# Performance work log

Hardware: AMD Instinct MI355X
Metric: run time of the kernel (lower is better)

The kernel has to match this reference:

```python
import jax, jax.numpy as jnp
import numpy as np

B_TAIL = 3.0  # 'bins' arg = tail bound of the spline interval [-B, B]


def _rqs_forward(u, w, h, d):
    """Rational-quadratic spline (Durkan et al.) with linear (identity) tails.
    u: (batch, dim); w,h: (dim, K); d: (dim, K-1). Returns x (batch, dim), logdet (batch,)."""
    dim, K = w.shape
    two_b = 2.0 * B_TAIL

    widths = jax.nn.softmax(w, axis=-1) * two_b                      # (dim, K)
    cum_w = jnp.concatenate(
        [jnp.full((dim, 1), -B_TAIL, u.dtype), -B_TAIL + jnp.cumsum(widths, axis=-1)],
        axis=-1)                                                     # (dim, K+1) knot x-positions
    cum_w = cum_w.at[:, -1].set(B_TAIL)

    heights = jax.nn.softmax(h, axis=-1) * two_b                     # (dim, K)
    cum_h = jnp.concatenate(
        [jnp.full((dim, 1), -B_TAIL, u.dtype), -B_TAIL + jnp.cumsum(heights, axis=-1)],
        axis=-1)                                                     # (dim, K+1) knot y-positions
    cum_h = cum_h.at[:, -1].set(B_TAIL)

    ones = jnp.ones((dim, 1), u.dtype)
    derivs = jnp.concatenate([ones, jax.nn.softplus(d), ones], axis=-1)  # (dim, K+1)

    inside = (u >= -B_TAIL) & (u <= B_TAIL)
    uc = jnp.clip(u, -B_TAIL, B_TAIL)

    # bin search: count interior knots <= uc  -> bin index in [0, K-1]
    idx = jnp.sum(uc[:, :, None] >= cum_w[None, :, 1:-1], axis=-1)   # (batch, dim) int32

    didx = jnp.arange(dim)[None, :]                                  # (1, dim)
    xk  = cum_w[didx, idx]
    wk  = widths[didx, idx]
    yk  = cum_h[didx, idx]
    hk  = heights[didx, idx]
    dk  = derivs[didx, idx]
    dk1 = derivs[didx, idx + 1]

    delta = hk / wk                                                  # bin slope
    theta = (uc - xk) / wk
    t1m = theta * (1.0 - theta)
    denom = delta + (dk + dk1 - 2.0 * delta) * t1m
    num = hk * (delta * theta * theta + dk * t1m)
    x_in = yk + num / denom

    ld_num = delta * delta * (dk1 * theta * theta + 2.0 * delta * t1m
                              + dk * (1.0 - theta) * (1.0 - theta))
    ld_in = jnp.log(ld_num) - 2.0 * jnp.log(denom)

    x = jnp.where(inside, x_in, u)          # identity linear tails
    ld = jnp.where(inside, ld_in, 0.0)
    return x, jnp.sum(ld, axis=-1)


def setup_inputs() -> dict:
    key = jax.random.key(0)
    ku, kw, kh, kd = jax.random.split(key, 4)
    batch, dim, K = 131072, 256, 5
    u = jax.random.normal(ku, (batch, dim), dtype=jnp.float32)
    w = jax.random.uniform(kw, (dim, K), dtype=jnp.float32, minval=-0.5, maxval=0.5)
    h = jax.random.uniform(kh, (dim, K), dtype=jnp.float32, minval=-0.5, maxval=0.5)
    d = jax.random.uniform(kd, (dim, K - 1), dtype=jnp.float32, minval=-0.5, maxval=0.5)
    return {"u": u, "w": w, "h": h, "d": d}


def reference(u, w, h, d):
    return _rqs_forward(u, w, h, d)
```

## Files before the change

kernel.cpp:

```cpp
#include <hip/hip_runtime.h>
#include <math.h>

#define BATCH 131072
#define DIM 256
#define NK 5
#define BT 3.0f
#define NBLK 1024
#define NTHR 512
#define ITERS 8

__global__ __launch_bounds__(NTHR, 8) void rqs_kernel(
    const float* __restrict__ u,
    const float* __restrict__ wp,
    const float* __restrict__ hp,
    const float* __restrict__ dp,
    float* __restrict__ x_out,
    float* __restrict__ ld_out)
{
    __shared__ float4 tab[NK * DIM * 2];
    const int tid = threadIdx.x;

    if (tid < DIM) {
        const int dm = tid;
        float v[NK], wid[NK], xpos[NK], hei[NK], ypos[NK], dv[NK + 1];
        float mx, sum, scale, c;

        mx = -1e30f;
        #pragma unroll
        for (int k = 0; k < NK; k++) { v[k] = wp[dm * NK + k]; mx = fmaxf(mx, v[k]); }
        sum = 0.f;
        #pragma unroll
        for (int k = 0; k < NK; k++) { v[k] = expf(v[k] - mx); sum += v[k]; }
        scale = 6.0f / sum;
        c = -BT;
        #pragma unroll
        for (int k = 0; k < NK; k++) { wid[k] = v[k] * scale; xpos[k] = c; c += wid[k]; }

        mx = -1e30f;
        #pragma unroll
        for (int k = 0; k < NK; k++) { v[k] = hp[dm * NK + k]; mx = fmaxf(mx, v[k]); }
        sum = 0.f;
        #pragma unroll
        for (int k = 0; k < NK; k++) { v[k] = expf(v[k] - mx); sum += v[k]; }
        scale = 6.0f / sum;
        c = -BT;
        #pragma unroll
        for (int k = 0; k < NK; k++) { hei[k] = v[k] * scale; ypos[k] = c; c += hei[k]; }

        dv[0] = 1.0f; dv[NK] = 1.0f;
        #pragma unroll
        for (int k = 0; k < 4; k++) dv[1 + k] = log1pf(expf(dp[dm * 4 + k]));

        #pragma unroll
        for (int k = 0; k < NK; k++) {
            float iw  = 1.0f / wid[k];
            float dlt = hei[k] * iw;
            float dk  = dv[k], dk1 = dv[k + 1];
            tab[2 * (k * DIM + dm)]     = make_float4(xpos[k], iw, dk + dk1 - 2.0f * dlt, dlt);
            tab[2 * (k * DIM + dm) + 1] = make_float4(hei[k] * (dlt - dk), hei[k] * dk,
                                                      ypos[k], 2.0f * (dlt - dk));
        }
    }
    __syncthreads();

    const int lane = tid & 63;
    const int wv   = tid >> 6;

    float kn[4][4];
    #pragma unroll
    for (int j = 0; j < 4; j++)
        #pragma unroll
        for (int i = 0; i < 4; i++)
            kn[j][i] = tab[2 * ((i + 1) * DIM + lane + 64 * j)].x;

    const int g = (blockIdx.x << 3) | wv;

    for (int it = 0; it < ITERS; it++) {
        const int r0 = (it << 14) | (g << 1);
        const float* up = u + (size_t)r0 * DIM + lane;

        float uin[2][4];
        #pragma unroll
        for (int rr = 0; rr < 2; rr++)
            #pragma unroll
            for (int j = 0; j < 4; j++)
                uin[rr][j] = up[rr * DIM + 64 * j];

        float lds[2] = {0.f, 0.f};
        #pragma unroll
        for (int rr = 0; rr < 2; rr++) {
            float xo[4];
            #pragma unroll
            for (int j = 0; j < 4; j++) {
                float uval = uin[rr][j];
                float uc = fminf(fmaxf(uval, -BT), BT);
                int idx = 0;
                idx += (uc >= kn[j][0]);
                idx += (uc >= kn[j][1]);
                idx += (uc >= kn[j][2]);
                idx += (uc >= kn[j][3]);
                const int a = 2 * (idx * DIM + lane + 64 * j);
                float4 A  = tab[a];
                float4 Bv = tab[a + 1];
                float xk = A.x, iw = A.y, s = A.z, dlt = A.w;
                float p = Bv.x, q = Bv.y, yk = Bv.z, rb = Bv.w;

                float th    = (uc - xk) * iw;
                float dk    = fmaf(-0.5f, rb, dlt);
                float r2    = dlt * dlt;
                float denom = fmaf(fmaf(-s, th, s), th, dlt);
                float invd  = __builtin_amdgcn_rcpf(denom);
                float num   = th * fmaf(p, th, q);
                float x_in  = fmaf(num, invd, yk);
                float ldq   = fmaf(fmaf(s, th, rb), th, dk);
                float ld    = __logf(ldq * r2 * invd * invd);

                xo[j] = (uc == uval) ? x_in : uval;
                lds[rr] += ld;
            }
            float* xp = x_out + (size_t)(r0 + rr) * DIM + lane;
            #pragma unroll
            for (int j = 0; j < 4; j++)
                __builtin_nontemporal_store(xo[j], xp + 64 * j);
        }

        #pragma unroll
        for (int off = 32; off > 0; off >>= 1) {
            lds[0] += __shfl_down(lds[0], off, 64);
            lds[1] += __shfl_down(lds[1], off, 64);
        }
        if (lane == 0) {
            __builtin_nontemporal_store(lds[0], ld_out + r0);
            __builtin_nontemporal_store(lds[1], ld_out + r0 + 1);
        }
    }
}

extern "C" void kernel_launch(void* const* d_in, const int* in_sizes, int n_in,
                              void* d_out, int out_size, void* d_ws, size_t ws_size,
                              hipStream_t stream) {
    const float* u  = (const float*)d_in[0];
    const float* w  = (const float*)d_in[1];
    const float* h  = (const float*)d_in[2];
    const float* dd = (const float*)d_in[3];
    float* x  = (float*)d_out;
    float* ld = x + (size_t)BATCH * DIM;
    rqs_kernel<<<NBLK, NTHR, 0, stream>>>(u, w, h, dd, x, ld);
}
```

Baseline: 244.9 us.

## Prefetch next iteration's inputs and split LDS table into two arrays

Software-pipelines the batch loop so each iteration issues global loads for the next iteration's rows before computing the current ones, hiding memory latency behind the spline math. The interleaved float4 table is split into two separate LDS arrays, and all table lookups for a row are gathered before any compute, which batches LDS reads. This adds register pressure under the 8-waves launch bound, which could reduce occupancy or cause spills.

New measurement: 283.3 us. 1.16x slower.

```diff
diff --git a/kernel.cpp b/kernel.cpp
--- a/kernel.cpp
+++ b/kernel.cpp
@@ -17,7 +17,8 @@
     float* __restrict__ x_out,
     float* __restrict__ ld_out)
 {
-    __shared__ float4 tab[NK * DIM * 2];
+    __shared__ float4 tabA[NK * DIM];
+    __shared__ float4 tabB[NK * DIM];
     const int tid = threadIdx.x;
 
     if (tid < DIM) {
@@ -56,9 +57,9 @@
             float iw  = 1.0f / wid[k];
             float dlt = hei[k] * iw;
             float dk  = dv[k], dk1 = dv[k + 1];
-            tab[2 * (k * DIM + dm)]     = make_float4(xpos[k], iw, dk + dk1 - 2.0f * dlt, dlt);
-            tab[2 * (k * DIM + dm) + 1] = make_float4(hei[k] * (dlt - dk), hei[k] * dk,
-                                                      ypos[k], 2.0f * (dlt - dk));
+            tabA[k * DIM + dm] = make_float4(xpos[k], iw, dk + dk1 - 2.0f * dlt, dlt);
+            tabB[k * DIM + dm] = make_float4(hei[k] * (dlt - dk), hei[k] * dk,
+                                             ypos[k], 2.0f * (dlt - dk));
         }
     }
     __syncthreads();
@@ -71,41 +72,60 @@
     for (int j = 0; j < 4; j++)
         #pragma unroll
         for (int i = 0; i < 4; i++)
-            kn[j][i] = tab[2 * ((i + 1) * DIM + lane + 64 * j)].x;
+            kn[j][i] = tabA[(i + 1) * DIM + lane + 64 * j].x;
 
     const int g = (blockIdx.x << 3) | wv;
 
-    for (int it = 0; it < ITERS; it++) {
-        const int r0 = (it << 14) | (g << 1);
-        const float* up = u + (size_t)r0 * DIM + lane;
-
-        float uin[2][4];
+    float uin[2][4];
+    {
+        const float* up = u + ((size_t)(g << 1)) * DIM + lane;
         #pragma unroll
         for (int rr = 0; rr < 2; rr++)
             #pragma unroll
             for (int j = 0; j < 4; j++)
                 uin[rr][j] = up[rr * DIM + 64 * j];
+    }
 
-        float lds[2] = {0.f, 0.f};
+    for (int it = 0; it < ITERS; it++) {
+        const int r0 = (it << 14) | (g << 1);
+
+        float unx[2][4];
+        if (it + 1 < ITERS) {
+            const float* up = u + ((size_t)(r0 + 16384)) * DIM + lane;
+            #pragma unroll
+            for (int rr = 0; rr < 2; rr++)
+                #pragma unroll
+                for (int j = 0; j < 4; j++)
+                    unx[rr][j] = up[rr * DIM + 64 * j];
+        }
+
+        float ldacc0 = 0.f, ldacc1 = 0.f;
+
         #pragma unroll
         for (int rr = 0; rr < 2; rr++) {
-            float xo[4];
+            float uc[4];
+            int   off[4];
             #pragma unroll
             for (int j = 0; j < 4; j++) {
                 float uval = uin[rr][j];
-                float uc = fminf(fmaxf(uval, -BT), BT);
-                int idx = 0;
-                idx += (uc >= kn[j][0]);
-                idx += (uc >= kn[j][1]);
-                idx += (uc >= kn[j][2]);
-                idx += (uc >= kn[j][3]);
-                const int a = 2 * (idx * DIM + lane + 64 * j);
-                float4 A  = tab[a];
-                float4 Bv = tab[a + 1];
-                float xk = A.x, iw = A.y, s = A.z, dlt = A.w;
-                float p = Bv.x, q = Bv.y, yk = Bv.z, rb = Bv.w;
+                float c = fminf(fmaxf(uval, -BT), BT);
+                int idx = (int)(c >= kn[j][0]) + (int)(c >= kn[j][1])
+                        + (int)(c >= kn[j][2]) + (int)(c >= kn[j][3]);
+                uc[j]  = c;
+                off[j] = (idx << 8) + lane + (j << 6);
+            }
+            float4 A[4], Bv[4];
+            #pragma unroll
+            for (int j = 0; j < 4; j++) { A[j] = tabA[off[j]]; Bv[j] = tabB[off[j]]; }
 
-                float th    = (uc - xk) * iw;
+            float xo[4];
+            float lsum = 0.f;
+            #pragma unroll
+            for (int j = 0; j < 4; j++) {
+                float xk = A[j].x,  iw = A[j].y,  s  = A[j].z,  dlt = A[j].w;
+                float p  = Bv[j].x, q  = Bv[j].y, yk = Bv[j].z, rb  = Bv[j].w;
+
+                float th    = (uc[j] - xk) * iw;
                 float dk    = fmaf(-0.5f, rb, dlt);
                 float r2    = dlt * dlt;
                 float denom = fmaf(fmaf(-s, th, s), th, dlt);
@@ -115,9 +135,11 @@
                 float ldq   = fmaf(fmaf(s, th, rb), th, dk);
                 float ld    = __logf(ldq * r2 * invd * invd);
 
-                xo[j] = (uc == uval) ? x_in : uval;
-                lds[rr] += ld;
+                xo[j] = (uc[j] == uin[rr][j]) ? x_in : uin[rr][j];
+                lsum += ld;
             }
+            if (rr == 0) ldacc0 = lsum; else ldacc1 = lsum;
+
             float* xp = x_out + (size_t)(r0 + rr) * DIM + lane;
             #pragma unroll
             for (int j = 0; j < 4; j++)
@@ -125,13 +147,21 @@
         }
 
         #pragma unroll
-        for (int off = 32; off > 0; off >>= 1) {
-            lds[0] += __shfl_down(lds[0], off, 64);
-            lds[1] += __shfl_down(lds[1], off, 64);
+        for (int sh = 32; sh > 0; sh >>= 1) {
+            ldacc0 += __shfl_down(ldacc0, sh, 64);
+            ldacc1 += __shfl_down(ldacc1, sh, 64);
         }
         if (lane == 0) {
-            __builtin_nontemporal_store(lds[0], ld_out + r0);
-            __builtin_nontemporal_store(lds[1], ld_out + r0 + 1);
+            __builtin_nontemporal_store(ldacc0, ld_out + r0);
+            __builtin_nontemporal_store(ldacc1, ld_out + r0 + 1);
+        }
+
+        if (it + 1 < ITERS) {
+            #pragma unroll
+            for (int rr = 0; rr < 2; rr++)
+                #pragma unroll
+                for (int j = 0; j < 4; j++)
+                    uin[rr][j] = unx[rr][j];
         }
     }
 }
```
